# Kernel tuning notes

Hardware: AMD Instinct MI355X
Metric: run time of the kernel (lower is better)

The kernel has to match this reference:

```python
import jax, jax.numpy as jnp
import numpy as np

SEQ_LEN, BATCH, INPUT_SIZE, HIDDEN, OUTPUT_SIZE = 100, 2048, 128, 512, 128
DEC_STEPS = 29


def lstm_cell(x, h, c, W_ih, W_hh, b_ih, b_hh):
    # torch LSTMCell gate order: i, f, g, o
    gates = x @ W_ih.T + b_ih + h @ W_hh.T + b_hh
    i, f, g, o = jnp.split(gates, 4, axis=-1)
    i = jax.nn.sigmoid(i)
    f = jax.nn.sigmoid(f)
    g = jnp.tanh(g)
    o = jax.nn.sigmoid(o)
    c_new = f * c + i * g
    h_new = o * jnp.tanh(c_new)
    return h_new, c_new


def setup_inputs() -> dict:
    key = jax.random.key(0)
    ks = jax.random.split(key, 10)
    s = 0.05
    return {
        "input": jax.random.normal(ks[0], (SEQ_LEN, BATCH, INPUT_SIZE), jnp.float32),
        "hidden_encoder": jnp.zeros((BATCH, HIDDEN), jnp.float32),
        "hidden_decoder": jnp.zeros((BATCH, HIDDEN), jnp.float32),
        "cell_encoder": jnp.zeros((BATCH, HIDDEN), jnp.float32),
        "cell_decoder": jnp.zeros((BATCH, HIDDEN), jnp.float32),
        "W_ih_enc": jax.random.normal(ks[1], (4 * HIDDEN, INPUT_SIZE), jnp.float32) * s,
        "W_hh_enc": jax.random.normal(ks[2], (4 * HIDDEN, HIDDEN), jnp.float32) * s,
        "b_ih_enc": jax.random.normal(ks[3], (4 * HIDDEN,), jnp.float32) * s,
        "b_hh_enc": jax.random.normal(ks[4], (4 * HIDDEN,), jnp.float32) * s,
        "W_ih_dec": jax.random.normal(ks[5], (4 * HIDDEN, HIDDEN), jnp.float32) * s,
        "W_hh_dec": jax.random.normal(ks[6], (4 * HIDDEN, HIDDEN), jnp.float32) * s,
        "b_ih_dec": jax.random.normal(ks[7], (4 * HIDDEN,), jnp.float32) * s,
        "b_hh_dec": jax.random.normal(ks[8], (4 * HIDDEN,), jnp.float32) * s,
        "W_lin": jax.random.normal(ks[9], (OUTPUT_SIZE, HIDDEN), jnp.float32) * s,
        "b_lin": jnp.zeros((OUTPUT_SIZE,), jnp.float32),
    }


def reference(input, hidden_encoder, hidden_decoder, cell_encoder, cell_decoder,
              W_ih_enc, W_hh_enc, b_ih_enc, b_hh_enc,
              W_ih_dec, W_hh_dec, b_ih_dec, b_hh_dec, W_lin, b_lin):
    # Encoder: sequential LSTMCell over time
    def enc_step(carry, x_t):
        h, c = carry
        h, c = lstm_cell(x_t, h, c, W_ih_enc, W_hh_enc, b_ih_enc, b_hh_enc)
        return (h, c), None

    (h_enc, c_enc), _ = jax.lax.scan(enc_step, (hidden_encoder, cell_encoder), input)

    # Decoder: 29 steps; input to the cell IS the current hidden state
    def dec_step(carry, _):
        h, c = carry
        h, c = lstm_cell(h, h, c, W_ih_dec, W_hh_dec, b_ih_dec, b_hh_dec)
        return (h, c), h

    (h_dec, c_dec), dec_hs = jax.lax.scan(dec_step, (h_enc, cell_decoder), None, length=DEC_STEPS)

    hs = jnp.concatenate([h_enc[None], dec_hs], axis=0)  # [30, B, H]
    output = hs @ W_lin.T + b_lin                         # [30, B, output_size]
    return (output, h_enc, h_dec, c_enc, c_dec)
```

## Files before the change

kernel.cpp:

```cpp
#include <hip/hip_runtime.h>

#define B_   2048
#define H_   512
#define I_   128
#define G4   2048
#define SEQ  100
#define DEC  29
#define OUT_ 128
#define TEAM 16

typedef __attribute__((ext_vector_type(8))) short bf16x8;
typedef __attribute__((ext_vector_type(4))) float f32x4;
typedef __attribute__((address_space(3))) unsigned int       lds_u32;
typedef __attribute__((address_space(1))) const unsigned int glb_u32c;

__device__ inline unsigned short f2bf(float f) {
    union { float f; unsigned int u; } v; v.f = f;
    unsigned int u = v.u + 0x7fffu + ((v.u >> 16) & 1u);
    return (unsigned short)(u >> 16);
}
__device__ inline float sigm(float x)  { return 1.f / (1.f + __expf(-x)); }
__device__ inline float tanh_(float x) { return 2.f / (1.f + __expf(-2.f * x)) - 1.f; }

template <int AUX>
__device__ inline void gl16(const unsigned short* g, unsigned short* l) {
    __builtin_amdgcn_global_load_lds((glb_u32c*)g, (lds_u32*)l, 16, 0, AUX);
}

__global__ __launch_bounds__(512, 2) void persist(
    const unsigned short* __restrict__ h0b,
    const unsigned short* __restrict__ xbf,
    const unsigned short* __restrict__ Wce,
    const unsigned short* __restrict__ Wd,
    const unsigned short* __restrict__ Wl,
    const float* __restrict__ be, const float* __restrict__ bd,
    const float* __restrict__ blin,
    const float* __restrict__ c_enc0, const float* __restrict__ c_dec0,
    unsigned short* __restrict__ hp0, unsigned short* __restrict__ hp1,
    unsigned short* __restrict__ hs,
    float* __restrict__ out_y,
    float* __restrict__ out_hEnc, float* __restrict__ out_cEnc,
    float* __restrict__ out_hDec, float* __restrict__ out_cDec,
    unsigned int* __restrict__ bar)
{
    __shared__ unsigned short smem[32768];

    const int tid  = threadIdx.x;
    const int b    = blockIdx.x;
    const int rg   = b & 15;
    const int cgB  = b >> 4;
    const int m0   = rg * 128;
    const int c0   = cgB * 32;

    const int lane = tid & 63, w = tid >> 6;
    const int quad = lane >> 4, l16 = lane & 15;
    const int w_m  = w >> 1, w_n = w & 1;

    unsigned int* bcnt = bar + rg * 64;
    unsigned int* bgen = bcnt + 32;
    unsigned int  my_gen = 0;

    const int  segl = (lane & 7) ^ ((lane >> 3) & 7);
    const bool isA  = (w < 4);
    const int  wS   = isA ? w : (w - 4);
    const int  sRow = wS * 32 + (lane >> 3);

    int offA[2][2], offB[4][2];
#pragma unroll
    for (int rf = 0; rf < 2; ++rf)
#pragma unroll
        for (int ks = 0; ks < 2; ++ks) {
            const int row = w_m * 32 + rf * 16 + l16;
            const int seg = ks * 4 + quad;
            offA[rf][ks] = row * 128 + ((seg ^ (row & 7)) * 16);
        }
#pragma unroll
    for (int g = 0; g < 4; ++g)
#pragma unroll
        for (int ks = 0; ks < 2; ++ks) {
            const int row = g * 32 + w_n * 16 + l16;
            const int seg = ks * 4 + quad;
            offB[g][ks] = 16384 + row * 128 + ((seg ^ (row & 7)) * 16);
        }

    f32x4 acc[2][4];
    float c_reg[2][4];
    const int col = c0 + w_n * 16 + l16;

    auto stage = [&](const unsigned short* Asrc, const unsigned short* Xsrc,
                     const unsigned short* Wsrc, int Kw, int gs, int cb,
                     int kc, int buf, bool coh) {
        unsigned short* dst = smem + buf * 16384 + (isA ? 0 : 8192) + wS * 2048;
        if (isA) {
            if (Xsrc && kc >= 8) {
                const unsigned short* g0 =
                    Xsrc + (size_t)(m0 + sRow) * I_ + (kc - 8) * 64 + segl * 8;
#pragma unroll
                for (int i = 0; i < 4; ++i)
                    gl16<0>(g0 + (size_t)(i * 8) * I_, dst + i * 512);
            } else {
                const unsigned short* g0 =
                    Asrc + (size_t)(m0 + sRow) * H_ + kc * 64 + segl * 8;
                if (coh) {
#pragma unroll
                    for (int i = 0; i < 4; ++i)
                        gl16<17>(g0 + (size_t)(i * 8) * H_, dst + i * 512);
                } else {
#pragma unroll
                    for (int i = 0; i < 4; ++i)
                        gl16<0>(g0 + (size_t)(i * 8) * H_, dst + i * 512);
                }
            }
        } else {
#pragma unroll
            for (int i = 0; i < 4; ++i) {
                const int rowN  = sRow + i * 8;
                const int rglob = (rowN >> 5) * gs + cb + (rowN & 31);
                gl16<0>(Wsrc + (size_t)rglob * Kw + kc * 64 + segl * 8, dst + i * 512);
            }
        }
    };

    auto gemm = [&](const unsigned short* Asrc, const unsigned short* Xsrc,
                    const unsigned short* Wsrc, int Kw, int gs, int cb, bool coh) {
#pragma unroll
        for (int rf = 0; rf < 2; ++rf)
#pragma unroll
            for (int g = 0; g < 4; ++g) acc[rf][g] = (f32x4){0.f, 0.f, 0.f, 0.f};
        const int kcN = Kw >> 6;
        stage(Asrc, Xsrc, Wsrc, Kw, gs, cb, 0, 0, coh);
        for (int kc = 0; kc < kcN; ++kc) {
            const int buf = kc & 1;
            __syncthreads();
            if (kc + 1 < kcN)
                stage(Asrc, Xsrc, Wsrc, Kw, gs, cb, kc + 1, buf ^ 1, coh);
            const char* sb = (const char*)smem + buf * 32768;
#pragma unroll
            for (int ks = 0; ks < 2; ++ks) {
                bf16x8 a0 = *(const bf16x8*)(sb + offA[0][ks]);
                bf16x8 a1 = *(const bf16x8*)(sb + offA[1][ks]);
#pragma unroll
                for (int g = 0; g < 4; ++g) {
                    bf16x8 bb = *(const bf16x8*)(sb + offB[g][ks]);
                    acc[0][g] = __builtin_amdgcn_mfma_f32_16x16x32_bf16(a0, bb, acc[0][g], 0, 0, 0);
                    acc[1][g] = __builtin_amdgcn_mfma_f32_16x16x32_bf16(a1, bb, acc[1][g], 0, 0, 0);
                }
            }
        }
        __syncthreads();
    };

    auto team_barrier = [&]() {
        __syncthreads();
        if (tid == 0) {
            unsigned old = __hip_atomic_fetch_add(bcnt, 1u, __ATOMIC_RELAXED,
                                                  __HIP_MEMORY_SCOPE_AGENT);
            if (old == (my_gen + 1u) * TEAM - 1u) {
                __hip_atomic_fetch_add(bgen, 1u, __ATOMIC_RELAXED,
                                       __HIP_MEMORY_SCOPE_AGENT);
            } else {
                while (__hip_atomic_load(bgen, __ATOMIC_RELAXED,
                                         __HIP_MEMORY_SCOPE_AGENT) <= my_gen)
                    __builtin_amdgcn_s_sleep(2);
            }
        }
        my_gen++;
        __syncthreads();
    };

    auto cell_epi = [&](float b0, float b1, float b2, float b3,
                        unsigned short* dst, float* hdump, float* cdump) {
        unsigned short* hstage = smem;
#pragma unroll
        for (int rf = 0; rf < 2; ++rf)
#pragma unroll
            for (int j = 0; j < 4; ++j) {
                const int row_l = w_m * 32 + rf * 16 + quad * 4 + j;
                const float gi = acc[rf][0][j] + b0;
                const float gf = acc[rf][1][j] + b1;
                const float gg = acc[rf][2][j] + b2;
                const float go = acc[rf][3][j] + b3;
                const float ii = sigm(gi), ff = sigm(gf);
                const float g2 = tanh_(gg), oo = sigm(go);
                const float cn = ff * c_reg[rf][j] + ii * g2;
                c_reg[rf][j] = cn;
                const float hn = oo * tanh_(cn);
                hstage[row_l * 32 + (w_n * 16 + l16)] = f2bf(hn);
                if (hdump) {
                    const size_t idx = (size_t)(m0 + row_l) * H_ + col;
                    hdump[idx] = hn; cdump[idx] = cn;
                }
            }
        __syncthreads();
        const unsigned int* h32 = (const unsigned int*)smem;
#pragma unroll
        for (int i = 0; i < 4; ++i) {
            const int idx = tid + i * 512;
            const int row = idx >> 4, cp = idx & 15;
            unsigned int* gp =
                (unsigned int*)(dst + (size_t)(m0 + row) * H_ + c0) + cp;
            __hip_atomic_store(gp, h32[idx], __ATOMIC_RELAXED,
                               __HIP_MEMORY_SCOPE_AGENT);
        }
    };

    {
        const float b0 = be[col], b1 = be[H_ + col],
                    b2 = be[2 * H_ + col], b3 = be[3 * H_ + col];
#pragma unroll
        for (int rf = 0; rf < 2; ++rf)
#pragma unroll
            for (int j = 0; j < 4; ++j) {
                const int row = m0 + w_m * 32 + rf * 16 + quad * 4 + j;
                c_reg[rf][j] = c_enc0[(size_t)row * H_ + col];
            }
        for (int t = 0; t < SEQ; ++t) {
            const unsigned short* src = (t == 0) ? h0b : ((t & 1) ? hp0 : hp1);
            unsigned short*       dst = (t == SEQ - 1) ? hs : ((t & 1) ? hp1 : hp0);
            const bool last = (t == SEQ - 1);
            gemm(src, xbf + (size_t)t * B_ * I_, Wce, 640, H_, c0, true);
            cell_epi(b0, b1, b2, b3, dst,
                     last ? out_hEnc : nullptr, last ? out_cEnc : nullptr);
            team_barrier();
        }
    }

    {
        const float b0 = bd[col], b1 = bd[H_ + col],
                    b2 = bd[2 * H_ + col], b3 = bd[3 * H_ + col];
#pragma unroll
        for (int rf = 0; rf < 2; ++rf)
#pragma unroll
            for (int j = 0; j < 4; ++j) {
                const int row = m0 + w_m * 32 + rf * 16 + quad * 4 + j;
                c_reg[rf][j] = c_dec0[(size_t)row * H_ + col];
            }
        for (int s = 0; s < DEC; ++s) {
            const bool last = (s == DEC - 1);
            gemm(hs + (size_t)s * B_ * H_, nullptr, Wd, 512, H_, c0, true);
            cell_epi(b0, b1, b2, b3, hs + (size_t)(s + 1) * B_ * H_,
                     last ? out_hDec : nullptr, last ? out_cDec : nullptr);
            team_barrier();
        }
    }

    for (int s = cgB; s < DEC + 1; s += 16) {
        gemm(hs + (size_t)s * B_ * H_, nullptr, Wl, 512, 32, 0, true);
#pragma unroll
        for (int g = 0; g < 4; ++g) {
            const int ocol = g * 32 + w_n * 16 + l16;
            const float bb = blin[ocol];
#pragma unroll
            for (int rf = 0; rf < 2; ++rf)
#pragma unroll
                for (int j = 0; j < 4; ++j) {
                    const int row = m0 + w_m * 32 + rf * 16 + quad * 4 + j;
                    out_y[(size_t)s * B_ * OUT_ + (size_t)row * OUT_ + ocol] =
                        acc[rf][g][j] + bb;
                }
        }
    }
}

__global__ void prep(const float* __restrict__ whh_e, const float* __restrict__ wih_e,
                     const float* __restrict__ wih_d, const float* __restrict__ whh_d,
                     const float* __restrict__ wlin,
                     const float* __restrict__ bie, const float* __restrict__ bhe,
                     const float* __restrict__ bid, const float* __restrict__ bhd,
                     unsigned short* __restrict__ Wce, unsigned short* __restrict__ Wd,
                     unsigned short* __restrict__ Wl,
                     float* __restrict__ be, float* __restrict__ bd)
{
    const int i = blockIdx.x * blockDim.x + threadIdx.x;
    if (i < G4 * 640) {
        const int r = i / 640, k = i % 640;
        Wce[i] = f2bf(k < H_ ? whh_e[r * H_ + k] : wih_e[r * I_ + (k - H_)]);
    }
    if (i < G4 * H_)   Wd[i] = f2bf(wih_d[i] + whh_d[i]);
    if (i < OUT_ * H_) Wl[i] = f2bf(wlin[i]);
    if (i < G4) { be[i] = bie[i] + bhe[i]; bd[i] = bid[i] + bhd[i]; }
}

__global__ void xconv(const float* __restrict__ x, unsigned short* __restrict__ xb, int n4)
{
    const int i = blockIdx.x * blockDim.x + threadIdx.x;
    if (i < n4) {
        const float4 f = *(const float4*)(x + (size_t)i * 4);
        ushort4 o;
        o.x = f2bf(f.x); o.y = f2bf(f.y); o.z = f2bf(f.z); o.w = f2bf(f.w);
        *(ushort4*)(xb + (size_t)i * 4) = o;
    }
}

__global__ void inith(const float* __restrict__ h0, unsigned short* __restrict__ hb)
{
    const int i = blockIdx.x * blockDim.x + threadIdx.x;
    if (i < B_ * H_) hb[i] = f2bf(h0[i]);
}

extern "C" void kernel_launch(void* const* d_in, const int* in_sizes, int n_in,
                              void* d_out, int out_size, void* d_ws, size_t ws_size,
                              hipStream_t stream) {
    (void)in_sizes; (void)n_in; (void)out_size; (void)ws_size;
    const float* input  = (const float*)d_in[0];
    const float* h_enc0 = (const float*)d_in[1];
    const float* c_enc0 = (const float*)d_in[3];
    const float* c_dec0 = (const float*)d_in[4];
    const float* Wih_e  = (const float*)d_in[5];
    const float* Whh_e  = (const float*)d_in[6];
    const float* bih_e  = (const float*)d_in[7];
    const float* bhh_e  = (const float*)d_in[8];
    const float* Wih_d  = (const float*)d_in[9];
    const float* Whh_d  = (const float*)d_in[10];
    const float* bih_d  = (const float*)d_in[11];
    const float* bhh_d  = (const float*)d_in[12];
    const float* Wlin   = (const float*)d_in[13];
    const float* blin   = (const float*)d_in[14];
    float* out = (float*)d_out;

    char* ws = (char*)d_ws;
    size_t off = 0;
    auto alloc = [&](size_t bytes) -> void* {
        void* p = ws + off;
        off = (off + bytes + 255) & ~(size_t)255;
        return p;
    };
    unsigned short* Wce = (unsigned short*)alloc((size_t)G4 * 640 * 2);
    unsigned short* Wd  = (unsigned short*)alloc((size_t)G4 * H_ * 2);
    unsigned short* Wl  = (unsigned short*)alloc((size_t)OUT_ * H_ * 2);
    float* be = (float*)alloc((size_t)G4 * 4);
    float* bd = (float*)alloc((size_t)G4 * 4);
    unsigned short* h0b = (unsigned short*)alloc((size_t)B_ * H_ * 2);
    unsigned short* hp0 = (unsigned short*)alloc((size_t)B_ * H_ * 2);
    unsigned short* hp1 = (unsigned short*)alloc((size_t)B_ * H_ * 2);
    unsigned short* xbf = (unsigned short*)alloc((size_t)SEQ * B_ * I_ * 2);
    unsigned short* hs  = (unsigned short*)alloc((size_t)(DEC + 1) * B_ * H_ * 2);
    unsigned int*   bar = (unsigned int*)alloc(16 * 64 * 4);

    float* out_y    = out;
    float* out_hEnc = out + (size_t)(DEC + 1) * B_ * OUT_;
    float* out_hDec = out_hEnc + (size_t)B_ * H_;
    float* out_cEnc = out_hDec + (size_t)B_ * H_;
    float* out_cDec = out_cEnc + (size_t)B_ * H_;

    prep<<<(G4 * 640 + 255) / 256, 256, 0, stream>>>(
        Whh_e, Wih_e, Wih_d, Whh_d, Wlin, bih_e, bhh_e, bih_d, bhh_d,
        Wce, Wd, Wl, be, bd);
    xconv<<<(SEQ * B_ * I_ / 4 + 255) / 256, 256, 0, stream>>>(input, xbf, SEQ * B_ * I_ / 4);
    inith<<<(B_ * H_ + 255) / 256, 256, 0, stream>>>(h_enc0, h0b);
    hipMemsetAsync(bar, 0, 16 * 64 * 4, stream);

    persist<<<256, 512, 0, stream>>>(
        h0b, xbf, Wce, Wd, Wl, be, bd, blin, c_enc0, c_dec0,
        hp0, hp1, hs, out_y, out_hEnc, out_cEnc, out_hDec, out_cDec, bar);
}
```

Baseline: 1.412 ms.

## Keep per-block weight slices in registers and stream only activations through LDS

Each block's slice of the recurrent and output weights is loaded once into registers (Bw) instead of being re-staged through LDS on every k-chunk of every timestep. Only the hidden/input activations go through a 4-deep LDS ring, with explicit vmcnt waits, raw s_barrier and raised wave priority around the MFMAs. The wave-to-tile mapping is reorganised so each lane holds two gate columns, and the i/f and g/o pairs are exchanged with lane shuffles in the cell epilogue. The aim is to cut LDS and global weight traffic on the serial critical path. The risk is that about 160 VGPRs of weights per thread, with launch_bounds(512,2), could spill to scratch or lower occupancy.

```diff
diff --git a/kernel.cpp b/kernel.cpp
--- a/kernel.cpp
+++ b/kernel.cpp
@@ -26,6 +26,10 @@
 __device__ inline void gl16(const unsigned short* g, unsigned short* l) {
     __builtin_amdgcn_global_load_lds((glb_u32c*)g, (lds_u32*)l, 16, 0, AUX);
 }
+
+#define WAIT_VM(n) asm volatile("s_waitcnt vmcnt(" #n ")" ::: "memory")
+
+template <int N> struct ic { static constexpr int v = N; };
 
 __global__ __launch_bounds__(512, 2) void persist(
     const unsigned short* __restrict__ h0b,
@@ -54,100 +58,101 @@
 
     const int lane = tid & 63, w = tid >> 6;
     const int quad = lane >> 4, l16 = lane & 15;
-    const int w_m  = w >> 1, w_n = w & 1;
+    const int bit3 = (lane >> 3) & 1;
+    const int co   = lane & 7;
+    const int wc   = w & 3;
+    const int rbase = (w >> 2) * 64;
+    const int jlo  = bit3 * 2;
+
+    const int hcl  = wc * 8 + co;
+    const int hcol = c0 + hcl;
 
     unsigned int* bcnt = bar + rg * 64;
     unsigned int* bgen = bcnt + 32;
     unsigned int  my_gen = 0;
 
-    const int  segl = (lane & 7) ^ ((lane >> 3) & 7);
-    const bool isA  = (w < 4);
-    const int  wS   = isA ? w : (w - 4);
-    const int  sRow = wS * 32 + (lane >> 3);
-
-    int offA[2][2], offB[4][2];
-#pragma unroll
-    for (int rf = 0; rf < 2; ++rf)
-#pragma unroll
-        for (int ks = 0; ks < 2; ++ks) {
-            const int row = w_m * 32 + rf * 16 + l16;
-            const int seg = ks * 4 + quad;
-            offA[rf][ks] = row * 128 + ((seg ^ (row & 7)) * 16);
-        }
-#pragma unroll
-    for (int g = 0; g < 4; ++g)
-#pragma unroll
-        for (int ks = 0; ks < 2; ++ks) {
-            const int row = g * 32 + w_n * 16 + l16;
-            const int seg = ks * 4 + quad;
-            offB[g][ks] = 16384 + row * 128 + ((seg ^ (row & 7)) * 16);
-        }
-
-    f32x4 acc[2][4];
-    float c_reg[2][4];
-    const int col = c0 + w_n * 16 + l16;
-
-    auto stage = [&](const unsigned short* Asrc, const unsigned short* Xsrc,
-                     const unsigned short* Wsrc, int Kw, int gs, int cb,
-                     int kc, int buf, bool coh) {
-        unsigned short* dst = smem + buf * 16384 + (isA ? 0 : 8192) + wS * 2048;
-        if (isA) {
-            if (Xsrc && kc >= 8) {
+    const int srow8 = lane >> 3;
+    const int segl  = co ^ srow8;
+
+    int lds_off[2];
+#pragma unroll
+    for (int ks = 0; ks < 2; ++ks)
+        lds_off[ks] = (rbase + l16) * 128 + (((ks * 4 + quad) ^ (lane & 7)) * 16);
+
+    bf16x8 Bw[2][20];
+    f32x4  acc[4][2];
+    float  c_reg[4][2];
+
+    auto loadB = [&](const unsigned short* W, int Kw, int GS, int cb, int nks) {
+#pragma unroll
+        for (int cf = 0; cf < 2; ++cf) {
+            const int grow = (cf * 2 + bit3) * GS + cb + hcl;
+            const unsigned short* wp = W + (size_t)grow * Kw + quad * 8;
+#pragma unroll
+            for (int ksg = 0; ksg < 20; ++ksg)
+                if (ksg < nks)
+                    Bw[cf][ksg] = *(const bf16x8*)(wp + ksg * 32);
+        }
+    };
+
+    auto gemm = [&](auto kcn_t, auto xt_t,
+                    const unsigned short* Asrc, const unsigned short* xsrc) {
+        constexpr int KCN = decltype(kcn_t)::v;
+        constexpr int XT  = decltype(xt_t)::v;
+
+        auto stg = [&](int kc, int buf, bool isx) {
+            unsigned short* dstl = smem + buf * 8192 + w * 1024;
+            if (isx) {
                 const unsigned short* g0 =
-                    Xsrc + (size_t)(m0 + sRow) * I_ + (kc - 8) * 64 + segl * 8;
-#pragma unroll
-                for (int i = 0; i < 4; ++i)
-                    gl16<0>(g0 + (size_t)(i * 8) * I_, dst + i * 512);
+                    xsrc + (m0 + w * 16 + srow8) * I_ + (kc - 8) * 64 + segl * 8;
+                gl16<0>(g0, dstl);
+                gl16<0>(g0 + 8 * I_, dstl + 512);
             } else {
                 const unsigned short* g0 =
-                    Asrc + (size_t)(m0 + sRow) * H_ + kc * 64 + segl * 8;
-                if (coh) {
-#pragma unroll
-                    for (int i = 0; i < 4; ++i)
-                        gl16<17>(g0 + (size_t)(i * 8) * H_, dst + i * 512);
-                } else {
-#pragma unroll
-                    for (int i = 0; i < 4; ++i)
-                        gl16<0>(g0 + (size_t)(i * 8) * H_, dst + i * 512);
-                }
-            }
-        } else {
-#pragma unroll
-            for (int i = 0; i < 4; ++i) {
-                const int rowN  = sRow + i * 8;
-                const int rglob = (rowN >> 5) * gs + cb + (rowN & 31);
-                gl16<0>(Wsrc + (size_t)rglob * Kw + kc * 64 + segl * 8, dst + i * 512);
-            }
-        }
-    };
-
-    auto gemm = [&](const unsigned short* Asrc, const unsigned short* Xsrc,
-                    const unsigned short* Wsrc, int Kw, int gs, int cb, bool coh) {
-#pragma unroll
-        for (int rf = 0; rf < 2; ++rf)
-#pragma unroll
-            for (int g = 0; g < 4; ++g) acc[rf][g] = (f32x4){0.f, 0.f, 0.f, 0.f};
-        const int kcN = Kw >> 6;
-        stage(Asrc, Xsrc, Wsrc, Kw, gs, cb, 0, 0, coh);
-        for (int kc = 0; kc < kcN; ++kc) {
-            const int buf = kc & 1;
-            __syncthreads();
-            if (kc + 1 < kcN)
-                stage(Asrc, Xsrc, Wsrc, Kw, gs, cb, kc + 1, buf ^ 1, coh);
-            const char* sb = (const char*)smem + buf * 32768;
+                    Asrc + (m0 + w * 16 + srow8) * H_ + kc * 64 + segl * 8;
+                gl16<17>(g0, dstl);
+                gl16<17>(g0 + 8 * H_, dstl + 512);
+            }
+        };
+
+#pragma unroll
+        for (int rf = 0; rf < 4; ++rf)
+#pragma unroll
+            for (int cf = 0; cf < 2; ++cf) acc[rf][cf] = (f32x4){0.f, 0.f, 0.f, 0.f};
+
+        __syncthreads();
+        stg(0, 0, false);
+        stg(1, 1, false);
+        stg(2, 2, false);
+#pragma unroll
+        for (int kc = 0; kc < KCN; ++kc) {
+            if (kc < KCN - 2)      { WAIT_VM(4); }
+            else if (kc == KCN - 2){ WAIT_VM(2); }
+            else                   { WAIT_VM(0); }
+            __builtin_amdgcn_s_barrier();
+            __builtin_amdgcn_sched_barrier(0);
+            if (kc + 3 < KCN) stg(kc + 3, (kc + 3) & 3, XT && (kc + 3) >= 8);
+
+            const char* sb = (const char*)smem + ((kc & 3) * 16384);
+            __builtin_amdgcn_s_setprio(1);
 #pragma unroll
             for (int ks = 0; ks < 2; ++ks) {
-                bf16x8 a0 = *(const bf16x8*)(sb + offA[0][ks]);
-                bf16x8 a1 = *(const bf16x8*)(sb + offA[1][ks]);
-#pragma unroll
-                for (int g = 0; g < 4; ++g) {
-                    bf16x8 bb = *(const bf16x8*)(sb + offB[g][ks]);
-                    acc[0][g] = __builtin_amdgcn_mfma_f32_16x16x32_bf16(a0, bb, acc[0][g], 0, 0, 0);
-                    acc[1][g] = __builtin_amdgcn_mfma_f32_16x16x32_bf16(a1, bb, acc[1][g], 0, 0, 0);
-                }
-            }
-        }
-        __syncthreads();
+                const int kk = kc * 2 + ks;
+                const bf16x8 a0 = *(const bf16x8*)(sb + lds_off[ks]);
+                const bf16x8 a1 = *(const bf16x8*)(sb + lds_off[ks] + 2048);
+                const bf16x8 a2 = *(const bf16x8*)(sb + lds_off[ks] + 4096);
+                const bf16x8 a3 = *(const bf16x8*)(sb + lds_off[ks] + 6144);
+                acc[0][0] = __builtin_amdgcn_mfma_f32_16x16x32_bf16(a0, Bw[0][kk], acc[0][0], 0, 0, 0);
+                acc[1][0] = __builtin_amdgcn_mfma_f32_16x16x32_bf16(a1, Bw[0][kk], acc[1][0], 0, 0, 0);
+                acc[2][0] = __builtin_amdgcn_mfma_f32_16x16x32_bf16(a2, Bw[0][kk], acc[2][0], 0, 0, 0);
+                acc[3][0] = __builtin_amdgcn_mfma_f32_16x16x32_bf16(a3, Bw[0][kk], acc[3][0], 0, 0, 0);
+                acc[0][1] = __builtin_amdgcn_mfma_f32_16x16x32_bf16(a0, Bw[1][kk], acc[0][1], 0, 0, 0);
+                acc[1][1] = __builtin_amdgcn_mfma_f32_16x16x32_bf16(a1, Bw[1][kk], acc[1][1], 0, 0, 0);
+                acc[2][1] = __builtin_amdgcn_mfma_f32_16x16x32_bf16(a2, Bw[1][kk], acc[2][1], 0, 0, 0);
+                acc[3][1] = __builtin_amdgcn_mfma_f32_16x16x32_bf16(a3, Bw[1][kk], acc[3][1], 0, 0, 0);
+            }
+            __builtin_amdgcn_s_setprio(0);
+        }
     };
 
     auto team_barrier = [&]() {
@@ -168,29 +173,38 @@
         __syncthreads();
     };
 
-    auto cell_epi = [&](float b0, float b1, float b2, float b3,
+    auto cell_epi = [&](float bi, float bf_, float bg, float bo,
                         unsigned short* dst, float* hdump, float* cdump) {
         unsigned short* hstage = smem;
 #pragma unroll
-        for (int rf = 0; rf < 2; ++rf)
-#pragma unroll
-            for (int j = 0; j < 4; ++j) {
-                const int row_l = w_m * 32 + rf * 16 + quad * 4 + j;
-                const float gi = acc[rf][0][j] + b0;
-                const float gf = acc[rf][1][j] + b1;
-                const float gg = acc[rf][2][j] + b2;
-                const float go = acc[rf][3][j] + b3;
+        for (int rf = 0; rf < 4; ++rf) {
+#pragma unroll
+            for (int jj = 0; jj < 2; ++jj) {
+                const float a0lo = acc[rf][0][jj],     a0hi = acc[rf][0][2 + jj];
+                const float a1lo = acc[rf][1][jj],     a1hi = acc[rf][1][2 + jj];
+                const float p0lo = __shfl_xor(a0lo, 8), p0hi = __shfl_xor(a0hi, 8);
+                const float p1lo = __shfl_xor(a1lo, 8), p1hi = __shfl_xor(a1hi, 8);
+                const float own0 = bit3 ? a0hi : a0lo;
+                const float own1 = bit3 ? a1hi : a1lo;
+                const float par0 = bit3 ? p0hi : p0lo;
+                const float par1 = bit3 ? p1hi : p1lo;
+                const float gi = (bit3 ? par0 : own0) + bi;
+                const float gf = (bit3 ? own0 : par0) + bf_;
+                const float gg = (bit3 ? par1 : own1) + bg;
+                const float go = (bit3 ? own1 : par1) + bo;
                 const float ii = sigm(gi), ff = sigm(gf);
                 const float g2 = tanh_(gg), oo = sigm(go);
-                const float cn = ff * c_reg[rf][j] + ii * g2;
-                c_reg[rf][j] = cn;
+                const float cn = ff * c_reg[rf][jj] + ii * g2;
+                c_reg[rf][jj] = cn;
                 const float hn = oo * tanh_(cn);
-                hstage[row_l * 32 + (w_n * 16 + l16)] = f2bf(hn);
+                const int row_l = rbase + rf * 16 + quad * 4 + jlo + jj;
+                hstage[row_l * 32 + hcl] = f2bf(hn);
                 if (hdump) {
-                    const size_t idx = (size_t)(m0 + row_l) * H_ + col;
+                    const size_t idx = (size_t)(m0 + row_l) * H_ + hcol;
                     hdump[idx] = hn; cdump[idx] = cn;
                 }
             }
+        }
         __syncthreads();
         const unsigned int* h32 = (const unsigned int*)smem;
 #pragma unroll
@@ -205,59 +219,64 @@
     };
 
     {
-        const float b0 = be[col], b1 = be[H_ + col],
-                    b2 = be[2 * H_ + col], b3 = be[3 * H_ + col];
-#pragma unroll
-        for (int rf = 0; rf < 2; ++rf)
-#pragma unroll
-            for (int j = 0; j < 4; ++j) {
-                const int row = m0 + w_m * 32 + rf * 16 + quad * 4 + j;
-                c_reg[rf][j] = c_enc0[(size_t)row * H_ + col];
+        loadB(Wce, 640, H_, c0, 20);
+        const float bi = be[hcol],            bf_ = be[H_ + hcol],
+                    bg = be[2 * H_ + hcol],   bo  = be[3 * H_ + hcol];
+#pragma unroll
+        for (int rf = 0; rf < 4; ++rf)
+#pragma unroll
+            for (int jj = 0; jj < 2; ++jj) {
+                const int row_l = rbase + rf * 16 + quad * 4 + jlo + jj;
+                c_reg[rf][jj] = c_enc0[(size_t)(m0 + row_l) * H_ + hcol];
             }
         for (int t = 0; t < SEQ; ++t) {
             const unsigned short* src = (t == 0) ? h0b : ((t & 1) ? hp0 : hp1);
             unsigned short*       dst = (t == SEQ - 1) ? hs : ((t & 1) ? hp1 : hp0);
             const bool last = (t == SEQ - 1);
-            gemm(src, xbf + (size_t)t * B_ * I_, Wce, 640, H_, c0, true);
-            cell_epi(b0, b1, b2, b3, dst,
+            gemm(ic<10>{}, ic<1>{}, src, xbf + (size_t)t * B_ * I_);
+            cell_epi(bi, bf_, bg, bo, dst,
                      last ? out_hEnc : nullptr, last ? out_cEnc : nullptr);
             team_barrier();
         }
     }
 
     {
-        const float b0 = bd[col], b1 = bd[H_ + col],
-                    b2 = bd[2 * H_ + col], b3 = bd[3 * H_ + col];
-#pragma unroll
-        for (int rf = 0; rf < 2; ++rf)
-#pragma unroll
-            for (int j = 0; j < 4; ++j) {
-                const int row = m0 + w_m * 32 + rf * 16 + quad * 4 + j;
-                c_reg[rf][j] = c_dec0[(size_t)row * H_ + col];
+        loadB(Wd, 512, H_, c0, 16);
+        const float bi = bd[hcol],            bf_ = bd[H_ + hcol],
+                    bg = bd[2 * H_ + hcol],   bo  = bd[3 * H_ + hcol];
+#pragma unroll
+        for (int rf = 0; rf < 4; ++rf)
+#pragma unroll
+            for (int jj = 0; jj < 2; ++jj) {
+                const int row_l = rbase + rf * 16 + quad * 4 + jlo + jj;
+                c_reg[rf][jj] = c_dec0[(size_t)(m0 + row_l) * H_ + hcol];
             }
         for (int s = 0; s < DEC; ++s) {
             const bool last = (s == DEC - 1);
-            gemm(hs + (size_t)s * B_ * H_, nullptr, Wd, 512, H_, c0, true);
-            cell_epi(b0, b1, b2, b3, hs + (size_t)(s + 1) * B_ * H_,
+            gemm(ic<8>{}, ic<0>{}, hs + (size_t)s * B_ * H_, nullptr);
+            cell_epi(bi, bf_, bg, bo, hs + (size_t)(s + 1) * B_ * H_,
                      last ? out_hDec : nullptr, last ? out_cDec : nullptr);
             team_barrier();
         }
     }
 
-    for (int s = cgB; s < DEC + 1; s += 16) {
-        gemm(hs + (size_t)s * B_ * H_, nullptr, Wl, 512, 32, 0, true);
-#pragma unroll
-        for (int g = 0; g < 4; ++g) {
-            const int ocol = g * 32 + w_n * 16 + l16;
-            const float bb = blin[ocol];
-#pragma unroll
-            for (int rf = 0; rf < 2; ++rf)
-#pragma unroll
-                for (int j = 0; j < 4; ++j) {
-                    const int row = m0 + w_m * 32 + rf * 16 + quad * 4 + j;
-                    out_y[(size_t)s * B_ * OUT_ + (size_t)row * OUT_ + ocol] =
-                        acc[rf][g][j] + bb;
-                }
+    {
+        loadB(Wl, 512, 32, 0, 16);
+        for (int s = cgB; s < DEC + 1; s += 16) {
+            gemm(ic<8>{}, ic<0>{}, hs + (size_t)s * B_ * H_, nullptr);
+#pragma unroll
+            for (int cf = 0; cf < 2; ++cf) {
+                const int oc = (cf * 2 + bit3) * 32 + hcl;
+                const float bbv = blin[oc];
+#pragma unroll
+                for (int rf = 0; rf < 4; ++rf)
+#pragma unroll
+                    for (int j = 0; j < 4; ++j) {
+                        const int row = m0 + rbase + rf * 16 + quad * 4 + j;
+                        out_y[(size_t)s * B_ * OUT_ + (size_t)row * OUT_ + oc] =
+                            acc[rf][cf][j] + bbv;
+                    }
+            }
         }
     }
 }
```

Result: faster. 1.276 ms (-9.7%).
